# Kernel tuning notes

Measured on AMD Instinct MI355X. Metric: run time of the kernel, lower is better.

The kernel has to match this reference:

```python
import jax, jax.numpy as jnp
import numpy as np

N, M, D, A = 10000, 32, 256, 128  # codes, max_ancestors(+self), embed dim, attention dim


def setup_inputs() -> dict:
    key = jax.random.key(0)
    k1, k2, k3, k4, k5 = jax.random.split(key, 5)
    basic_embeddings = jax.random.normal(k1, (N, D), jnp.float32) * 0.1
    # padded ancestry table; slot 0 is the code itself (diagonal filled in original)
    code_ancestry = jax.random.randint(k2, (N, M), 0, N)
    code_ancestry = code_ancestry.at[:, 0].set(jnp.arange(N))
    # variable-length valid prefix per code, like the original padding scheme
    lengths = jax.random.randint(k3, (N,), 1, M + 1)
    code_ancestry_mask = (jnp.arange(M)[None, :] < lengths[:, None]).astype(jnp.float32)
    Wp = jax.random.normal(k4, (A, 2 * D), jnp.float32) / np.float32(np.sqrt(2 * D))
    bp = jnp.zeros((A,), jnp.float32)
    Ww = jax.random.normal(k5, (1, A), jnp.float32) / np.float32(np.sqrt(A))
    return {
        "basic_embeddings": basic_embeddings,
        "code_ancestry": code_ancestry,
        "code_ancestry_mask": code_ancestry_mask,
        "Wp": Wp,
        "bp": bp,
        "Ww": Ww,
    }


def reference(basic_embeddings, code_ancestry, code_ancestry_mask, Wp, bp, Ww):
    # GRAM.ancestry_attention vmapped over all codes (compute_embeddings_mat with all-ones in_vec).
    d = basic_embeddings.shape[1]
    Wp_self, Wp_anc = Wp[:, :d], Wp[:, d:]  # hstack((e_i, e_j)) split: e_i part, ancestor part
    E = basic_embeddings[code_ancestry]  # [N, M, D] gathered ancestor embeddings
    # DAGAttention: weighted_sum(tanh(project(concat(e_i, e_j))))
    self_proj = basic_embeddings @ Wp_self.T              # [N, A]
    anc_proj = jnp.einsum('nmd,ad->nma', E, Wp_anc)       # [N, M, A]
    h = jnp.tanh(self_proj[:, None, :] + anc_proj + bp)   # [N, M, A]
    scores = jnp.einsum('nma,a->nm', h, Ww[0])            # [N, M]
    A_att = scores * code_ancestry_mask
    # unnormalized_softmax weights, then jnp.average over ancestors
    w = jnp.exp(A_att - jax.lax.stop_gradient(A_att.max(axis=-1, keepdims=True)))  # [N, M]
    G = jnp.einsum('nm,nmd->nd', w, E) / w.sum(axis=-1, keepdims=True)             # [N, D]
    return G
```

## Files before the change

### kernel.cpp

```cpp
#include <hip/hip_runtime.h>
#include <hip/hip_bf16.h>

#define NROW 10000
#define MANC 32
#define DIM  256
#define ADIM 128

typedef __attribute__((ext_vector_type(8))) short short8;
typedef __attribute__((ext_vector_type(4))) short short4v;
typedef __attribute__((ext_vector_type(4))) float floatx4;

__device__ __forceinline__ short f2bf(float x) {
    union { __hip_bfloat16 h; short s; } u;
    u.h = __float2bfloat16(x);
    return u.s;
}
__device__ __forceinline__ float bf2f(unsigned short u) {
    unsigned int x = ((unsigned int)u) << 16;
    return __uint_as_float(x);
}

__global__ __launch_bounds__(256) void cvt_kernel(
    const float* __restrict__ be, const float* __restrict__ Wp,
    __hip_bfloat16* __restrict__ beb, __hip_bfloat16* __restrict__ w2b) {
    int tid = blockIdx.x * 256 + threadIdx.x;
    const float* src;
    short* dst;
    if (tid < 640000) {
        int base = tid * 4;
        src = be + base;
        dst = reinterpret_cast<short*>(beb) + base;
    } else {
        int base = (tid - 640000) * 4;
        int j = base >> 8;
        int k = base & 255;
        src = (j < ADIM) ? (Wp + j * (2 * DIM) + k)
                         : (Wp + (j - ADIM) * (2 * DIM) + DIM + k);
        dst = reinterpret_cast<short*>(w2b) + base;
    }
    floatx4 v = *reinterpret_cast<const floatx4*>(src);
    short4v s;
#pragma unroll
    for (int e = 0; e < 4; ++e) s[e] = f2bf(v[e]);
    *reinterpret_cast<short4v*>(dst) = s;
}

__global__ __launch_bounds__(256) void proj_kernel(
    const __hip_bfloat16* __restrict__ beb, const __hip_bfloat16* __restrict__ w2b,
    __hip_bfloat16* __restrict__ SP) {
    int wid = (blockIdx.x << 2) + (threadIdx.x >> 6);
    int l   = threadIdx.x & 63;
    int tm  = wid >> 2;
    int q   = wid & 3;
    int kc  = (l >> 4) * 8;

    const unsigned short* A = reinterpret_cast<const unsigned short*>(beb)
                              + (size_t)(tm * 16 + (l & 15)) * DIM;
    const unsigned short* B = reinterpret_cast<const unsigned short*>(w2b);
    int c0 = q * 64 + (l & 15);

    floatx4 acc[4] = {{0,0,0,0},{0,0,0,0},{0,0,0,0},{0,0,0,0}};
#pragma unroll
    for (int k0 = 0; k0 < DIM; k0 += 32) {
        short8 av = *reinterpret_cast<const short8*>(A + k0 + kc);
#pragma unroll
        for (int t = 0; t < 4; ++t) {
            short8 bv = *reinterpret_cast<const short8*>(
                B + (size_t)(c0 + t * 16) * DIM + k0 + kc);
            acc[t] = __builtin_amdgcn_mfma_f32_16x16x32_bf16(av, bv, acc[t], 0, 0, 0);
        }
    }
    int orow = tm * 16 + ((l >> 4) << 2);
#pragma unroll
    for (int t = 0; t < 4; ++t) {
#pragma unroll
        for (int r = 0; r < 4; ++r) {
            union { __hip_bfloat16 h; short s; } u;
            u.s = f2bf(acc[t][r]);
            SP[(size_t)(orow + r) * DIM + q * 64 + t * 16 + (l & 15)] = u.h;
        }
    }
}

__global__ __launch_bounds__(256) void attn_kernel(
    const int*   __restrict__ anc,
    const float* __restrict__ mask,
    const float* __restrict__ bias,
    const float* __restrict__ Ww,
    const __hip_bfloat16* __restrict__ SP,
    const __hip_bfloat16* __restrict__ beb,
    float* __restrict__ out) {
    int tid = blockIdx.x * 256 + threadIdx.x;
    int l   = tid & 63;
    int n   = __builtin_amdgcn_readfirstlane(tid >> 6);
    int kc  = (l >> 4) * 8;

    const unsigned short* SPu = reinterpret_cast<const unsigned short*>(SP);

    float ssb[4][8];
#pragma unroll
    for (int kt = 0; kt < 4; ++kt) {
        short8 sv = *reinterpret_cast<const short8*>(SPu + (size_t)n * DIM + kt * 32 + kc);
        floatx4 b0 = *reinterpret_cast<const floatx4*>(bias + kt * 32 + kc);
        floatx4 b1 = *reinterpret_cast<const floatx4*>(bias + kt * 32 + kc + 4);
#pragma unroll
        for (int i = 0; i < 8; ++i)
            ssb[kt][i] = bf2f((unsigned short)sv[i]) + ((i < 4) ? b0[i & 3] : b1[i & 3]);
    }

    float keep = ((l & 15) == 0) ? 1.f : 0.f;
    short8 bw[4];
#pragma unroll
    for (int kt = 0; kt < 4; ++kt) {
        floatx4 w0 = *reinterpret_cast<const floatx4*>(Ww + kt * 32 + kc);
        floatx4 w1 = *reinterpret_cast<const floatx4*>(Ww + kt * 32 + kc + 4);
#pragma unroll
        for (int i = 0; i < 8; ++i)
            bw[kt][i] = f2bf(((i < 4) ? w0[i & 3] : w1[i & 3]) * keep);
    }

    int m0 = l & 15;
    int j0 = anc[n * MANC + m0];
    int j1 = anc[n * MANC + 16 + m0];

    floatx4 acc0 = {0,0,0,0}, acc1 = {0,0,0,0};
#pragma unroll
    for (int kt = 0; kt < 4; ++kt) {
        short8 pv = *reinterpret_cast<const short8*>(
            SPu + (size_t)j0 * DIM + ADIM + kt * 32 + kc);
        short8 af;
#pragma unroll
        for (int i = 0; i < 8; ++i) {
            float x  = ssb[kt][i] + bf2f((unsigned short)pv[i]);
            float x2 = __builtin_amdgcn_fmed3f(x + x, -16.f, 16.f);
            float e  = __expf(x2);
            af[i]    = f2bf((e - 1.f) * __builtin_amdgcn_rcpf(e + 1.f));
        }
        acc0 = __builtin_amdgcn_mfma_f32_16x16x32_bf16(af, bw[kt], acc0, 0, 0, 0);
    }
#pragma unroll
    for (int kt = 0; kt < 4; ++kt) {
        short8 pv = *reinterpret_cast<const short8*>(
            SPu + (size_t)j1 * DIM + ADIM + kt * 32 + kc);
        short8 af;
#pragma unroll
        for (int i = 0; i < 8; ++i) {
            float x  = ssb[kt][i] + bf2f((unsigned short)pv[i]);
            float x2 = __builtin_amdgcn_fmed3f(x + x, -16.f, 16.f);
            float e  = __expf(x2);
            af[i]    = f2bf((e - 1.f) * __builtin_amdgcn_rcpf(e + 1.f));
        }
        acc1 = __builtin_amdgcn_mfma_f32_16x16x32_bf16(af, bw[kt], acc1, 0, 0, 0);
    }

    int rb = (l >> 4) << 2;
    float s0[4], s1[4];
#pragma unroll
    for (int r = 0; r < 4; ++r) {
        s0[r] = acc0[r] * mask[n * MANC + rb + r];
        s1[r] = acc1[r] * mask[n * MANC + 16 + rb + r];
    }
    float mx = s0[0];
#pragma unroll
    for (int r = 0; r < 4; ++r) { mx = fmaxf(mx, s0[r]); mx = fmaxf(mx, s1[r]); }
    mx = fmaxf(mx, __shfl_xor(mx, 16, 64));
    mx = fmaxf(mx, __shfl_xor(mx, 32, 64));
    float wn0[4], wn1[4], tot = 0.f;
#pragma unroll
    for (int r = 0; r < 4; ++r) {
        wn0[r] = __expf(s0[r] - mx); tot += wn0[r];
        wn1[r] = __expf(s1[r] - mx); tot += wn1[r];
    }
    tot += __shfl_xor(tot, 16, 64);
    tot += __shfl_xor(tot, 32, 64);
    float inv = __builtin_amdgcn_rcpf(tot);
#pragma unroll
    for (int r = 0; r < 4; ++r) { wn0[r] *= inv; wn1[r] *= inv; }

    const unsigned short* bebu = reinterpret_cast<const unsigned short*>(beb);
    floatx4 acc = {0,0,0,0};
#pragma unroll
    for (int m = 0; m < MANC; ++m) {
        int src = ((m & 15) >> 2) << 4;
        float wm = (m < 16) ? __shfl(wn0[m & 3], src, 64)
                            : __shfl(wn1[m & 3], src, 64);
        int j = anc[n * MANC + m];
        short4v ev = *reinterpret_cast<const short4v*>(bebu + (size_t)j * DIM + l * 4);
#pragma unroll
        for (int e = 0; e < 4; ++e) acc[e] += wm * bf2f((unsigned short)ev[e]);
    }
    *reinterpret_cast<floatx4*>(out + (size_t)n * DIM + l * 4) = acc;
}

extern "C" void kernel_launch(void* const* d_in, const int* in_sizes, int n_in,
                              void* d_out, int out_size, void* d_ws, size_t ws_size,
                              hipStream_t stream) {
    const float* be   = (const float*)d_in[0];
    const int*   anc  = (const int*)d_in[1];
    const float* mask = (const float*)d_in[2];
    const float* Wp   = (const float*)d_in[3];
    const float* bias = (const float*)d_in[4];
    const float* Ww   = (const float*)d_in[5];
    float* out = (float*)d_out;

    __hip_bfloat16* SPb = (__hip_bfloat16*)d_ws;
    __hip_bfloat16* beb = (__hip_bfloat16*)((char*)d_ws + (size_t)NROW * DIM * 2);
    __hip_bfloat16* w2b = (__hip_bfloat16*)((char*)d_ws + (size_t)2 * NROW * DIM * 2);

    cvt_kernel<<<2564, 256, 0, stream>>>(be, Wp, beb, w2b);
    proj_kernel<<<625, 256, 0, stream>>>(beb, w2b, SPb);
    attn_kernel<<<2500, 256, 0, stream>>>(anc, mask, bias, Ww, SPb, beb, out);
}
```

Measured before the change: 56.76 us.

## Fuse bf16 conversion into projection GEMM with LDS weights, skip masked second tile

Removes the separate conversion kernel. The projection kernel now converts fp32 embeddings to bf16 on the fly, writes the bf16 copy once, and stages the bf16 weight slice in swizzled LDS per block. The attention kernel rewrites tanh and softmax with exp2 and folded constants, and skips the second 16-ancestor score tile when mask slot 16 is zero. It also defers the normalization to a single multiply at the end. The aim is to save a launch and a global round trip plus transcendental work, at the cost of LDS use and a wave-uniform branch.

```diff
diff --git a/kernel.cpp b/kernel.cpp
--- a/kernel.cpp
+++ b/kernel.cpp
@@ -9,77 +9,111 @@
 typedef __attribute__((ext_vector_type(8))) short short8;
 typedef __attribute__((ext_vector_type(4))) short short4v;
 typedef __attribute__((ext_vector_type(4))) float floatx4;
-
-__device__ __forceinline__ short f2bf(float x) {
+typedef __attribute__((ext_vector_type(2))) unsigned int uint2v;
+
+#if __has_builtin(__builtin_amdgcn_exp2f)
+#define EXP2F(x) __builtin_amdgcn_exp2f(x)
+#else
+#define EXP2F(x) __expf((x) * 0.69314718055994531f)
+#endif
+
+#define C2L2E 2.8853900817779268f
+#define L2E   1.4426950408889634f
+
+static __device__ __forceinline__ short f2bf(float x) {
     union { __hip_bfloat16 h; short s; } u;
     u.h = __float2bfloat16(x);
     return u.s;
 }
-__device__ __forceinline__ float bf2f(unsigned short u) {
-    unsigned int x = ((unsigned int)u) << 16;
-    return __uint_as_float(x);
-}
-
-__global__ __launch_bounds__(256) void cvt_kernel(
+static __device__ __forceinline__ float bf2f(unsigned short u) {
+    return __uint_as_float(((unsigned int)u) << 16);
+}
+
+__global__ __launch_bounds__(256) void proj_kernel(
     const float* __restrict__ be, const float* __restrict__ Wp,
-    __hip_bfloat16* __restrict__ beb, __hip_bfloat16* __restrict__ w2b) {
-    int tid = blockIdx.x * 256 + threadIdx.x;
-    const float* src;
-    short* dst;
-    if (tid < 640000) {
-        int base = tid * 4;
-        src = be + base;
-        dst = reinterpret_cast<short*>(beb) + base;
-    } else {
-        int base = (tid - 640000) * 4;
-        int j = base >> 8;
-        int k = base & 255;
-        src = (j < ADIM) ? (Wp + j * (2 * DIM) + k)
-                         : (Wp + (j - ADIM) * (2 * DIM) + DIM + k);
-        dst = reinterpret_cast<short*>(w2b) + base;
-    }
-    floatx4 v = *reinterpret_cast<const floatx4*>(src);
-    short4v s;
-#pragma unroll
-    for (int e = 0; e < 4; ++e) s[e] = f2bf(v[e]);
-    *reinterpret_cast<short4v*>(dst) = s;
-}
-
-__global__ __launch_bounds__(256) void proj_kernel(
-    const __hip_bfloat16* __restrict__ beb, const __hip_bfloat16* __restrict__ w2b,
-    __hip_bfloat16* __restrict__ SP) {
-    int wid = (blockIdx.x << 2) + (threadIdx.x >> 6);
-    int l   = threadIdx.x & 63;
-    int tm  = wid >> 2;
-    int q   = wid & 3;
-    int kc  = (l >> 4) * 8;
-
-    const unsigned short* A = reinterpret_cast<const unsigned short*>(beb)
-                              + (size_t)(tm * 16 + (l & 15)) * DIM;
-    const unsigned short* B = reinterpret_cast<const unsigned short*>(w2b);
-    int c0 = q * 64 + (l & 15);
+    __hip_bfloat16* __restrict__ SP, __hip_bfloat16* __restrict__ beb) {
+    __shared__ short lds[64 * 256];
+    int q  = blockIdx.x & 3;
+    int rb = blockIdx.x >> 2;
+    int t  = threadIdx.x;
+
+#pragma unroll
+    for (int i = 0; i < 8; ++i) {
+        int c  = i * 256 + t;
+        int jl = c >> 5;
+        int e0 = (c & 31) * 8;
+        int j  = q * 64 + jl;
+        const float* src = (j < ADIM) ? (Wp + (size_t)j * (2 * DIM) + e0)
+                                      : (Wp + (size_t)(j - ADIM) * (2 * DIM) + DIM + e0);
+        floatx4 v0 = *(const floatx4*)src;
+        floatx4 v1 = *(const floatx4*)(src + 4);
+        short8 s;
+#pragma unroll
+        for (int e = 0; e < 4; ++e) { s[e] = f2bf(v0[e]); s[4 + e] = f2bf(v1[e]); }
+        int byte = (c * 16) ^ ((jl & 7) << 4);
+        *(short8*)((char*)lds + byte) = s;
+    }
+    __syncthreads();
+
+    int w    = t >> 6;
+    int l    = t & 63;
+    int tm   = rb * 4 + w;
+    int arow = tm * 16 + (l & 15);
+    int rcl  = min(arow, NROW - 1);
+    int kc   = (l >> 4) * 8;
+    const float* A = be + (size_t)rcl * DIM;
 
     floatx4 acc[4] = {{0,0,0,0},{0,0,0,0},{0,0,0,0},{0,0,0,0}};
 #pragma unroll
     for (int k0 = 0; k0 < DIM; k0 += 32) {
-        short8 av = *reinterpret_cast<const short8*>(A + k0 + kc);
-#pragma unroll
-        for (int t = 0; t < 4; ++t) {
-            short8 bv = *reinterpret_cast<const short8*>(
-                B + (size_t)(c0 + t * 16) * DIM + k0 + kc);
-            acc[t] = __builtin_amdgcn_mfma_f32_16x16x32_bf16(av, bv, acc[t], 0, 0, 0);
+        floatx4 a0 = *(const floatx4*)(A + k0 + kc);
+        floatx4 a1 = *(const floatx4*)(A + k0 + kc + 4);
+        short8 av;
+#pragma unroll
+        for (int e = 0; e < 4; ++e) { av[e] = f2bf(a0[e]); av[4 + e] = f2bf(a1[e]); }
+        if (q == 0 && arow < NROW)
+            *(short8*)((unsigned short*)beb + (size_t)arow * DIM + k0 + kc) = av;
+#pragma unroll
+        for (int tt = 0; tt < 4; ++tt) {
+            int jl   = tt * 16 + (l & 15);
+            int byte = (jl * 512 + (k0 + kc) * 2) ^ ((jl & 7) << 4);
+            short8 bv = *(const short8*)((char*)lds + byte);
+            acc[tt] = __builtin_amdgcn_mfma_f32_16x16x32_bf16(av, bv, acc[tt], 0, 0, 0);
         }
     }
     int orow = tm * 16 + ((l >> 4) << 2);
 #pragma unroll
-    for (int t = 0; t < 4; ++t) {
+    for (int tt = 0; tt < 4; ++tt) {
 #pragma unroll
         for (int r = 0; r < 4; ++r) {
-            union { __hip_bfloat16 h; short s; } u;
-            u.s = f2bf(acc[t][r]);
-            SP[(size_t)(orow + r) * DIM + q * 64 + t * 16 + (l & 15)] = u.h;
+            if (orow + r < NROW) {
+                union { __hip_bfloat16 h; short s; } u;
+                u.s = f2bf(acc[tt][r]);
+                SP[(size_t)(orow + r) * DIM + q * 64 + tt * 16 + (l & 15)] = u.h;
+            }
         }
     }
+}
+
+static __device__ __forceinline__ floatx4 score_tile(
+    const unsigned short* __restrict__ SPu, int j, int kc,
+    const float (&ssby)[4][8], const short8 (&bw)[4], floatx4 acc) {
+    const unsigned short* p = SPu + (size_t)j * DIM + ADIM + kc;
+#pragma unroll
+    for (int kt = 0; kt < 4; ++kt) {
+        short8 pv = *(const short8*)(p + kt * 32);
+        short8 af;
+#pragma unroll
+        for (int i = 0; i < 8; ++i) {
+            float y = fmaf(bf2f((unsigned short)pv[i]), C2L2E, ssby[kt][i]);
+            y = __builtin_amdgcn_fmed3f(y, -28.f, 28.f);
+            float e = EXP2F(y);
+            float r = __builtin_amdgcn_rcpf(e + 1.f);
+            af[i] = f2bf(fmaf(-2.f, r, 1.f));
+        }
+        acc = __builtin_amdgcn_mfma_f32_16x16x32_bf16(af, bw[kt], acc, 0, 0, 0);
+    }
+    return acc;
 }
 
 __global__ __launch_bounds__(256) void attn_kernel(
@@ -94,102 +128,79 @@
     int l   = tid & 63;
     int n   = __builtin_amdgcn_readfirstlane(tid >> 6);
     int kc  = (l >> 4) * 8;
-
-    const unsigned short* SPu = reinterpret_cast<const unsigned short*>(SP);
-
-    float ssb[4][8];
+    const unsigned short* SPu = (const unsigned short*)SP;
+
+    float ssby[4][8];
 #pragma unroll
     for (int kt = 0; kt < 4; ++kt) {
-        short8 sv = *reinterpret_cast<const short8*>(SPu + (size_t)n * DIM + kt * 32 + kc);
-        floatx4 b0 = *reinterpret_cast<const floatx4*>(bias + kt * 32 + kc);
-        floatx4 b1 = *reinterpret_cast<const floatx4*>(bias + kt * 32 + kc + 4);
+        short8 sv = *(const short8*)(SPu + (size_t)n * DIM + kt * 32 + kc);
+        floatx4 b0 = *(const floatx4*)(bias + kt * 32 + kc);
+        floatx4 b1 = *(const floatx4*)(bias + kt * 32 + kc + 4);
 #pragma unroll
         for (int i = 0; i < 8; ++i)
-            ssb[kt][i] = bf2f((unsigned short)sv[i]) + ((i < 4) ? b0[i & 3] : b1[i & 3]);
+            ssby[kt][i] = (bf2f((unsigned short)sv[i]) + ((i < 4) ? b0[i & 3] : b1[i & 3])) * C2L2E;
     }
 
     float keep = ((l & 15) == 0) ? 1.f : 0.f;
     short8 bw[4];
 #pragma unroll
     for (int kt = 0; kt < 4; ++kt) {
-        floatx4 w0 = *reinterpret_cast<const floatx4*>(Ww + kt * 32 + kc);
-        floatx4 w1 = *reinterpret_cast<const floatx4*>(Ww + kt * 32 + kc + 4);
+        floatx4 w0 = *(const floatx4*)(Ww + kt * 32 + kc);
+        floatx4 w1 = *(const floatx4*)(Ww + kt * 32 + kc + 4);
 #pragma unroll
         for (int i = 0; i < 8; ++i)
             bw[kt][i] = f2bf(((i < 4) ? w0[i & 3] : w1[i & 3]) * keep);
     }
 
+    const int*   ancn = anc  + n * MANC;
+    const float* mrow = mask + n * MANC;
+    bool has2 = mrow[16] != 0.f;
+
     int m0 = l & 15;
-    int j0 = anc[n * MANC + m0];
-    int j1 = anc[n * MANC + 16 + m0];
-
     floatx4 acc0 = {0,0,0,0}, acc1 = {0,0,0,0};
-#pragma unroll
-    for (int kt = 0; kt < 4; ++kt) {
-        short8 pv = *reinterpret_cast<const short8*>(
-            SPu + (size_t)j0 * DIM + ADIM + kt * 32 + kc);
-        short8 af;
-#pragma unroll
-        for (int i = 0; i < 8; ++i) {
-            float x  = ssb[kt][i] + bf2f((unsigned short)pv[i]);
-            float x2 = __builtin_amdgcn_fmed3f(x + x, -16.f, 16.f);
-            float e  = __expf(x2);
-            af[i]    = f2bf((e - 1.f) * __builtin_amdgcn_rcpf(e + 1.f));
-        }
-        acc0 = __builtin_amdgcn_mfma_f32_16x16x32_bf16(af, bw[kt], acc0, 0, 0, 0);
-    }
-#pragma unroll
-    for (int kt = 0; kt < 4; ++kt) {
-        short8 pv = *reinterpret_cast<const short8*>(
-            SPu + (size_t)j1 * DIM + ADIM + kt * 32 + kc);
-        short8 af;
-#pragma unroll
-        for (int i = 0; i < 8; ++i) {
-            float x  = ssb[kt][i] + bf2f((unsigned short)pv[i]);
-            float x2 = __builtin_amdgcn_fmed3f(x + x, -16.f, 16.f);
-            float e  = __expf(x2);
-            af[i]    = f2bf((e - 1.f) * __builtin_amdgcn_rcpf(e + 1.f));
-        }
-        acc1 = __builtin_amdgcn_mfma_f32_16x16x32_bf16(af, bw[kt], acc1, 0, 0, 0);
-    }
+    acc0 = score_tile(SPu, ancn[m0], kc, ssby, bw, acc0);
+    if (has2)
+        acc1 = score_tile(SPu, ancn[16 + m0], kc, ssby, bw, acc1);
 
     int rb = (l >> 4) << 2;
     float s0[4], s1[4];
 #pragma unroll
     for (int r = 0; r < 4; ++r) {
-        s0[r] = acc0[r] * mask[n * MANC + rb + r];
-        s1[r] = acc1[r] * mask[n * MANC + 16 + rb + r];
+        s0[r] = acc0[r] * mrow[rb + r];
+        s1[r] = acc1[r] * mrow[16 + rb + r];
     }
     float mx = s0[0];
 #pragma unroll
     for (int r = 0; r < 4; ++r) { mx = fmaxf(mx, s0[r]); mx = fmaxf(mx, s1[r]); }
     mx = fmaxf(mx, __shfl_xor(mx, 16, 64));
     mx = fmaxf(mx, __shfl_xor(mx, 32, 64));
+    float nm = -mx * L2E;
     float wn0[4], wn1[4], tot = 0.f;
 #pragma unroll
     for (int r = 0; r < 4; ++r) {
-        wn0[r] = __expf(s0[r] - mx); tot += wn0[r];
-        wn1[r] = __expf(s1[r] - mx); tot += wn1[r];
+        wn0[r] = EXP2F(fmaf(s0[r], L2E, nm)); tot += wn0[r];
+        wn1[r] = EXP2F(fmaf(s1[r], L2E, nm)); tot += wn1[r];
     }
     tot += __shfl_xor(tot, 16, 64);
     tot += __shfl_xor(tot, 32, 64);
+    tot = __shfl(tot, 0, 64);
     float inv = __builtin_amdgcn_rcpf(tot);
-#pragma unroll
-    for (int r = 0; r < 4; ++r) { wn0[r] *= inv; wn1[r] *= inv; }
-
-    const unsigned short* bebu = reinterpret_cast<const unsigned short*>(beb);
-    floatx4 acc = {0,0,0,0};
+
+    const unsigned short* ebase = (const unsigned short*)beb + (size_t)l * 4;
+    float a0 = 0.f, a1 = 0.f, a2 = 0.f, a3 = 0.f;
 #pragma unroll
     for (int m = 0; m < MANC; ++m) {
         int src = ((m & 15) >> 2) << 4;
         float wm = (m < 16) ? __shfl(wn0[m & 3], src, 64)
                             : __shfl(wn1[m & 3], src, 64);
-        int j = anc[n * MANC + m];
-        short4v ev = *reinterpret_cast<const short4v*>(bebu + (size_t)j * DIM + l * 4);
-#pragma unroll
-        for (int e = 0; e < 4; ++e) acc[e] += wm * bf2f((unsigned short)ev[e]);
-    }
-    *reinterpret_cast<floatx4*>(out + (size_t)n * DIM + l * 4) = acc;
+        uint2v dv = *(const uint2v*)(ebase + (size_t)ancn[m] * DIM);
+        a0 = fmaf(wm, __uint_as_float(dv.x << 16),          a0);
+        a1 = fmaf(wm, __uint_as_float(dv.x & 0xffff0000u),  a1);
+        a2 = fmaf(wm, __uint_as_float(dv.y << 16),          a2);
+        a3 = fmaf(wm, __uint_as_float(dv.y & 0xffff0000u),  a3);
+    }
+    floatx4 res = {a0 * inv, a1 * inv, a2 * inv, a3 * inv};
+    *(floatx4*)(out + (size_t)n * DIM + l * 4) = res;
 }
 
 extern "C" void kernel_launch(void* const* d_in, const int* in_sizes, int n_in,
@@ -205,9 +216,7 @@
 
     __hip_bfloat16* SPb = (__hip_bfloat16*)d_ws;
     __hip_bfloat16* beb = (__hip_bfloat16*)((char*)d_ws + (size_t)NROW * DIM * 2);
-    __hip_bfloat16* w2b = (__hip_bfloat16*)((char*)d_ws + (size_t)2 * NROW * DIM * 2);
-
-    cvt_kernel<<<2564, 256, 0, stream>>>(be, Wp, beb, w2b);
-    proj_kernel<<<625, 256, 0, stream>>>(beb, w2b, SPb);
+
+    proj_kernel<<<628, 256, 0, stream>>>(be, Wp, SPb, beb);
     attn_kernel<<<2500, 256, 0, stream>>>(anc, mask, bias, Ww, SPb, beb, out);
 }
```

Measured after the change: 46.69 us. -17.7%, faster.
